# Kernel tuning notes

Hardware: AMD Instinct MI355X
Metric: run time of the kernel (lower is better)

## Reference

```python
import jax, jax.numpy as jnp
import numpy as np

B, T, C, F, E, K = 4, 2048, 1024, 4096, 8, 2
CAP_FACTOR = 1.0
AUX_COEF = 0.01
CAPACITY = max(1, int(CAP_FACTOR * (B * T) * max(1, K) / E + 0.9999))


def setup_inputs() -> dict:
    key = jax.random.key(0)
    ks = jax.random.split(key, 4)
    s = 0.02
    return {
        "x": jax.random.normal(ks[0], (B, T, C), jnp.float32),
        "w_gate": jax.random.normal(ks[1], (C, E), jnp.float32) * s,
        "b_gate": jnp.zeros((E,), jnp.float32),
        "W1": jax.random.normal(ks[2], (E, C, F), jnp.float32) * s,
        "b1": jnp.zeros((E, F), jnp.float32),
        "W2": jax.random.normal(ks[3], (E, F, C), jnp.float32) * s,
        "b2": jnp.zeros((E, C), jnp.float32),
    }


def reference(x, w_gate, b_gate, W1, b1, W2, b2):
    Bb, Tt, Cc = x.shape
    N = Bb * Tt
    S = N * K  # dispatch slots, token-major with k inner (matches the python double loop order)
    x_flat = x.reshape(N, Cc)

    # Top-K gating
    logits = x_flat @ w_gate + b_gate                       # [N, E]
    probs = jax.nn.softmax(logits, axis=-1)
    topk_w, topk_idx = jax.lax.top_k(probs, K)              # [N, K]
    topk_w = topk_w / (topk_w.sum(-1, keepdims=True) + 1e-9)

    e_flat = topk_idx.reshape(S)                            # expert id per slot
    w_flat = topk_w.reshape(S)
    tok = jnp.arange(S) // K                                # source token per slot

    # First-come-first-served capacity: position of each slot within its expert
    onehot = jax.nn.one_hot(e_flat, E, dtype=jnp.int32)     # [S, E]
    pos_in_e = (jnp.cumsum(onehot, axis=0) - onehot)        # exclusive count per expert
    pos_in_e = (pos_in_e * onehot).sum(-1)                  # [S]
    keep = pos_in_e < CAPACITY
    keepf = keep.astype(x.dtype)
    p_safe = jnp.where(keep, pos_in_e, CAPACITY - 1)        # dropped slots scatter zeros

    # Dispatch -> [E, capacity, C]
    disp = jnp.zeros((E, CAPACITY, Cc), x.dtype).at[e_flat, p_safe].add(
        x_flat[tok] * keepf[:, None]
    )

    # Per-expert FFN (grouped GEMM)
    h = jax.nn.gelu(jnp.einsum("epc,ecf->epf", disp, W1) + b1[:, None, :])
    y = jnp.einsum("epf,efc->epc", h, W2) + b2[:, None, :]  # [E, capacity, C]

    # Combine: gather each kept slot's expert output, weight, scatter-add back to tokens
    y_slot = y[e_flat, p_safe] * (w_flat * keepf)[:, None]  # [S, C]
    out = jnp.zeros((N, Cc), x.dtype).at[tok].add(y_slot).reshape(Bb, Tt, Cc)

    # Load-balancing aux loss (expert_load is detached in the original)
    expert_load = jnp.sum(onehot.astype(jnp.float32) * keepf[:, None], axis=0)  # [E]
    expert_load = jax.lax.stop_gradient(expert_load)
    frac_expected = probs.mean(axis=0)
    frac_expected = frac_expected / (frac_expected.sum() + 1e-9)
    frac_actual = expert_load / (expert_load.sum() + 1e-9)
    aux_loss = AUX_COEF * jnp.mean((frac_expected - frac_actual) ** 2)

    return out, aux_loss
```

## Files before the change

kernel.cpp:

```cpp
#include <hip/hip_runtime.h>
#include <hip/hip_bf16.h>
#include <math.h>


#define DEV __device__ __forceinline__

typedef __attribute__((ext_vector_type(4))) float f32x4;
typedef __attribute__((ext_vector_type(8))) short bf16x8;

constexpr int B_ = 4, T_ = 2048, C_ = 1024, F_ = 4096, E_ = 8, TOPK_ = 2;
constexpr int N_ = B_ * T_;
constexpr int S_ = N_ * TOPK_;
constexpr int CAP_ = 2048;

#define GLOAD16(G, L)                                              \
  __builtin_amdgcn_global_load_lds(                                \
      (const __attribute__((address_space(1))) void*)(G),          \
      (__attribute__((address_space(3))) void*)(L), 16, 0, 0)

DEV float gelu_tanh(float x) {
  float x3 = x * x * x;
  float u = 0.7978845608028654f * (x + 0.044715f * x3);
  return 0.5f * x * (1.0f + tanhf(u));
}


__global__ __launch_bounds__(256) void cvt_x_kernel(
    const float* __restrict__ in, __hip_bfloat16* __restrict__ out, int n4) {
  int i = blockIdx.x * 256 + threadIdx.x;
  if (i >= n4) return;
  float4 v = ((const float4*)in)[i];
  __hip_bfloat16 o[4] = {__float2bfloat16(v.x), __float2bfloat16(v.y),
                         __float2bfloat16(v.z), __float2bfloat16(v.w)};
  *(uint2*)(out + (size_t)i * 4) = *(uint2*)o;
}

__global__ __launch_bounds__(256) void transpose_cvt_kernel(
    const float* __restrict__ in, __hip_bfloat16* __restrict__ out, int R, int S) {
  __shared__ float tile[32][33];
  int e = blockIdx.z;
  int s0 = blockIdx.x * 32;
  int r0 = blockIdx.y * 32;
  int tx = threadIdx.x & 31;
  int ty = threadIdx.x >> 5;
  const float* ip = in + (size_t)e * R * S;
  __hip_bfloat16* op = out + (size_t)e * R * S;
#pragma unroll
  for (int i = 0; i < 32; i += 8)
    tile[ty + i][tx] = ip[(size_t)(r0 + ty + i) * S + s0 + tx];
  __syncthreads();
#pragma unroll
  for (int i = 0; i < 32; i += 8)
    op[(size_t)(s0 + ty + i) * R + r0 + tx] = __float2bfloat16(tile[tx][ty + i]);
}


__global__ __launch_bounds__(256) void gate_kernel(
    const float* __restrict__ x, const float* __restrict__ wg,
    const float* __restrict__ bg, int* __restrict__ slot_e,
    float* __restrict__ slot_w, float* __restrict__ probs_sum) {
  int lane = threadIdx.x & 63;
  int wv = threadIdx.x >> 6;
  int wid = blockIdx.x * 4 + wv;
  float psum[E_];
#pragma unroll
  for (int e = 0; e < E_; ++e) psum[e] = 0.f;

  for (int ti = 0; ti < 8; ++ti) {
    int t = wid * 8 + ti;
    const float* xr = x + (size_t)t * C_;
    float acc[E_];
#pragma unroll
    for (int e = 0; e < E_; ++e) acc[e] = 0.f;
    for (int c = lane; c < C_; c += 64) {
      float xv = xr[c];
      const float* wr = wg + (size_t)c * E_;
#pragma unroll
      for (int e = 0; e < E_; ++e) acc[e] += xv * wr[e];
    }
#pragma unroll
    for (int e = 0; e < E_; ++e) {
#pragma unroll
      for (int off = 32; off >= 1; off >>= 1)
        acc[e] += __shfl_xor(acc[e], off, 64);
    }
    if (lane == 0) {
      float lg[E_], p[E_];
      float mx = -1e30f;
#pragma unroll
      for (int e = 0; e < E_; ++e) { lg[e] = acc[e] + bg[e]; mx = fmaxf(mx, lg[e]); }
      float s = 0.f;
#pragma unroll
      for (int e = 0; e < E_; ++e) { p[e] = expf(lg[e] - mx); s += p[e]; }
      float inv = 1.f / s;
#pragma unroll
      for (int e = 0; e < E_; ++e) { p[e] *= inv; psum[e] += p[e]; }
      int i1 = 0; float p1 = p[0];
#pragma unroll
      for (int e = 1; e < E_; ++e) if (p[e] > p1) { p1 = p[e]; i1 = e; }
      int i2 = -1; float p2 = -1.f;
#pragma unroll
      for (int e = 0; e < E_; ++e) if (e != i1 && p[e] > p2) { p2 = p[e]; i2 = e; }
      float wden = 1.f / (p1 + p2 + 1e-9f);
      slot_e[2 * t] = i1;     slot_w[2 * t] = p1 * wden;
      slot_e[2 * t + 1] = i2; slot_w[2 * t + 1] = p2 * wden;
    }
  }
  if (lane == 0) {
#pragma unroll
    for (int e = 0; e < E_; ++e) atomicAdd(&probs_sum[e], psum[e]);
  }
}


__global__ __launch_bounds__(256) void scan_kernel(
    const int* __restrict__ slot_e, const float* __restrict__ slot_w,
    int* __restrict__ idx_list, float* __restrict__ w_list,
    const float* __restrict__ probs_sum, float* __restrict__ aux_out) {
  __shared__ int sc[256][E_];
  int tid = threadIdx.x;
  int s0 = tid * 64;
  int cnt[E_];
#pragma unroll
  for (int e = 0; e < E_; ++e) cnt[e] = 0;
  for (int j = 0; j < 64; ++j) cnt[slot_e[s0 + j]]++;
#pragma unroll
  for (int e = 0; e < E_; ++e) sc[tid][e] = cnt[e];
  __syncthreads();
  for (int off = 1; off < 256; off <<= 1) {
    int v[E_];
    bool act = (tid >= off);
    if (act) {
#pragma unroll
      for (int e = 0; e < E_; ++e) v[e] = sc[tid - off][e];
    }
    __syncthreads();
    if (act) {
#pragma unroll
      for (int e = 0; e < E_; ++e) sc[tid][e] += v[e];
    }
    __syncthreads();
  }
  int base[E_];
#pragma unroll
  for (int e = 0; e < E_; ++e) base[e] = tid ? sc[tid - 1][e] : 0;
  for (int j = 0; j < 64; ++j) {
    int s = s0 + j;
    int e = slot_e[s];
    int p = base[e]++;
    if (p < CAP_) {
      idx_list[e * CAP_ + p] = s >> 1;
      w_list[e * CAP_ + p] = slot_w[s];
    }
  }
  if (tid == 0) {
    float fe[E_], fa[E_], fs = 0.f, ls = 0.f;
#pragma unroll
    for (int e = 0; e < E_; ++e) {
      fe[e] = probs_sum[e] / (float)N_;
      fs += fe[e];
      int tot = sc[255][e];
      fa[e] = (float)(tot < CAP_ ? tot : CAP_);
      ls += fa[e];
    }
    float i1 = 1.f / (fs + 1e-9f), i2 = 1.f / (ls + 1e-9f);
    float a = 0.f;
#pragma unroll
    for (int e = 0; e < E_; ++e) {
      float d = fe[e] * i1 - fa[e] * i2;
      a += d * d;
    }
    aux_out[0] = 0.01f * a / (float)E_;
  }
}


template <int EPI, bool GATHER>
__global__ __launch_bounds__(256) void gemm_tile(
    const __hip_bfloat16* __restrict__ Aall,
    const __hip_bfloat16* __restrict__ Ball,
    const int* __restrict__ idxl,
    const float* __restrict__ wl,
    const float* __restrict__ bias,
    void* __restrict__ Cout,
    const __hip_bfloat16* __restrict__ zrow,
    int Ndim, int Kdim) {
  const int e = blockIdx.z;
  const int row0 = blockIdx.y * 128;
  const int col0 = blockIdx.x * 128;
  const int tid = threadIdx.x;
  const int lane = tid & 63;
  const int wv = tid >> 6;
  const int wm = wv >> 1, wn = wv & 1;

  __shared__ __align__(16) __hip_bfloat16 As[128 * 32];
  __shared__ __align__(16) __hip_bfloat16 Bs[128 * 32];

  const int rA0 = tid >> 2, kA0 = (tid & 3) * 8;
  const int rA1 = rA0 + 64;

  const __hip_bfloat16 *rowA0, *rowA1;
  if (GATHER) {
    int tok0 = idxl[e * CAP_ + row0 + rA0];
    int tok1 = idxl[e * CAP_ + row0 + rA1];
    rowA0 = (tok0 >= 0) ? Aall + (size_t)tok0 * Kdim : zrow;
    rowA1 = (tok1 >= 0) ? Aall + (size_t)tok1 * Kdim : zrow;
  } else {
    rowA0 = Aall + ((size_t)e * CAP_ + row0 + rA0) * Kdim;
    rowA1 = Aall + ((size_t)e * CAP_ + row0 + rA1) * Kdim;
  }
  const __hip_bfloat16* Be = Ball + (size_t)e * Ndim * Kdim;
  const __hip_bfloat16* rowB0 = Be + (size_t)(col0 + rA0) * Kdim;
  const __hip_bfloat16* rowB1 = Be + (size_t)(col0 + rA1) * Kdim;

  __hip_bfloat16* ldsA0 = As + (size_t)(wv * 64) * 8;
  __hip_bfloat16* ldsA1 = As + (size_t)(256 + wv * 64) * 8;
  __hip_bfloat16* ldsB0 = Bs + (size_t)(wv * 64) * 8;
  __hip_bfloat16* ldsB1 = Bs + (size_t)(256 + wv * 64) * 8;

  f32x4 acc[4][4];
#pragma unroll
  for (int m = 0; m < 4; ++m)
#pragma unroll
    for (int n = 0; n < 4; ++n) acc[m][n] = (f32x4){0.f, 0.f, 0.f, 0.f};

  const int rsel = lane & 15;
  const int ksel = (lane >> 4) * 8;

  for (int k0 = 0; k0 < Kdim; k0 += 32) {
    GLOAD16(rowA0 + k0 + kA0, ldsA0);
    GLOAD16(rowA1 + k0 + kA0, ldsA1);
    GLOAD16(rowB0 + k0 + kA0, ldsB0);
    GLOAD16(rowB1 + k0 + kA0, ldsB1);
    __syncthreads();

    bf16x8 af[4], bfv[4];
#pragma unroll
    for (int m = 0; m < 4; ++m)
      af[m] = *(const bf16x8*)(As + (wm * 64 + m * 16 + rsel) * 32 + ksel);
#pragma unroll
    for (int n = 0; n < 4; ++n)
      bfv[n] = *(const bf16x8*)(Bs + (wn * 64 + n * 16 + rsel) * 32 + ksel);
#pragma unroll
    for (int m = 0; m < 4; ++m)
#pragma unroll
      for (int n = 0; n < 4; ++n)
        acc[m][n] = __builtin_amdgcn_mfma_f32_16x16x32_bf16(af[m], bfv[n],
                                                            acc[m][n], 0, 0, 0);
    __syncthreads();
  }

  const float* brow = bias + (size_t)e * Ndim;
  const int orow0 = row0 + wm * 64 + (lane >> 4) * 4;
  const int ocol0 = col0 + wn * 64 + rsel;
  if (EPI == 0) {
    __hip_bfloat16* H = (__hip_bfloat16*)Cout + (size_t)e * CAP_ * Ndim;
#pragma unroll
    for (int m = 0; m < 4; ++m) {
#pragma unroll
      for (int n = 0; n < 4; ++n) {
        int cc = ocol0 + n * 16;
        float bv = brow[cc];
#pragma unroll
        for (int j = 0; j < 4; ++j) {
          int rr = orow0 + m * 16 + j;
          H[(size_t)rr * Ndim + cc] = __float2bfloat16(gelu_tanh(acc[m][n][j] + bv));
        }
      }
    }
  } else {
    float* out = (float*)Cout;
#pragma unroll
    for (int m = 0; m < 4; ++m) {
#pragma unroll
      for (int j = 0; j < 4; ++j) {
        int rr = orow0 + m * 16 + j;
        int t = idxl[e * CAP_ + rr];
        if (t < 0) continue;
        float w = wl[e * CAP_ + rr];
#pragma unroll
        for (int n = 0; n < 4; ++n) {
          int cc = ocol0 + n * 16;
          unsafeAtomicAdd(&out[(size_t)t * C_ + cc], w * (acc[m][n][j] + brow[cc]));
        }
      }
    }
  }
}


extern "C" void kernel_launch(void* const* d_in, const int* in_sizes, int n_in,
                              void* d_out, int out_size, void* d_ws,
                              size_t ws_size, hipStream_t stream) {
  (void)in_sizes; (void)n_in; (void)out_size; (void)ws_size;
  const float* x = (const float*)d_in[0];
  const float* w_gate = (const float*)d_in[1];
  const float* b_gate = (const float*)d_in[2];
  const float* W1 = (const float*)d_in[3];
  const float* b1 = (const float*)d_in[4];
  const float* W2 = (const float*)d_in[5];
  const float* b2 = (const float*)d_in[6];
  float* out = (float*)d_out;

  char* p = (char*)d_ws;
  __hip_bfloat16* xb = (__hip_bfloat16*)p;
  __hip_bfloat16* W1t = (__hip_bfloat16*)(p + ((size_t)16 << 20));
  __hip_bfloat16* W2t = (__hip_bfloat16*)p;
  __hip_bfloat16* Hb = (__hip_bfloat16*)(p + ((size_t)80 << 20));
  char* meta = p + ((size_t)208 << 20);
  int* slot_e = (int*)meta;
  float* slot_w = (float*)(meta + (64 << 10));
  int* idx_list = (int*)(meta + (128 << 10));
  float* w_list = (float*)(meta + (192 << 10));
  float* probs_sum = (float*)(meta + (256 << 10));
  __hip_bfloat16* zrow = (__hip_bfloat16*)(meta + (260 << 10));

  hipMemsetAsync(idx_list, 0xFF, E_ * CAP_ * sizeof(int), stream);
  hipMemsetAsync(probs_sum, 0, E_ * sizeof(float), stream);
  hipMemsetAsync(zrow, 0, 16 << 10, stream);
  hipMemsetAsync(out, 0, (size_t)N_ * C_ * sizeof(float), stream);

  cvt_x_kernel<<<(N_ * C_ / 4 + 255) / 256, 256, 0, stream>>>(x, xb, N_ * C_ / 4);
  transpose_cvt_kernel<<<dim3(F_ / 32, C_ / 32, E_), 256, 0, stream>>>(W1, W1t, C_, F_);
  gate_kernel<<<N_ / 32, 256, 0, stream>>>(x, w_gate, b_gate, slot_e, slot_w, probs_sum);
  scan_kernel<<<1, 256, 0, stream>>>(slot_e, slot_w, idx_list, w_list, probs_sum,
                                     out + (size_t)N_ * C_);
  gemm_tile<0, true><<<dim3(F_ / 128, CAP_ / 128, E_), 256, 0, stream>>>(
      xb, W1t, idx_list, nullptr, b1, Hb, zrow, F_, C_);
  transpose_cvt_kernel<<<dim3(C_ / 32, F_ / 32, E_), 256, 0, stream>>>(W2, W2t, F_, C_);
  gemm_tile<1, false><<<dim3(C_ / 128, CAP_ / 128, E_), 256, 0, stream>>>(
      Hb, W2t, idx_list, w_list, b2, out, zrow, C_, F_);
}
```

Before: 1.089 ms.

## Replace 128x128 grouped GEMM with double-buffered 256x256 tiles and swizzled LDS

Both expert GEMMs now use 256x256 output tiles with 512 threads and a K step of 64. Each wave computes 128x64 from double-buffered LDS, prefetching the next tile while MFMAs run on the current one. LDS reads use an XOR swizzle to avoid bank conflicts, wave priority is raised around the MFMA bursts, and a block-index remap places workgroups across XCDs. The aim is more data reuse per load and load latency hidden behind compute, at the cost of 128KB of LDS per block, higher register pressure, and fewer blocks per expert for the second GEMM.

```diff
diff --git a/kernel.cpp b/kernel.cpp
--- a/kernel.cpp
+++ b/kernel.cpp
@@ -176,7 +176,7 @@
 
 
 template <int EPI, bool GATHER>
-__global__ __launch_bounds__(256) void gemm_tile(
+__global__ __launch_bounds__(512, 2) void gemm256(
     const __hip_bfloat16* __restrict__ Aall,
     const __hip_bfloat16* __restrict__ Ball,
     const int* __restrict__ idxl,
@@ -184,107 +184,143 @@
     const float* __restrict__ bias,
     void* __restrict__ Cout,
     const __hip_bfloat16* __restrict__ zrow,
-    int Ndim, int Kdim) {
-  const int e = blockIdx.z;
-  const int row0 = blockIdx.y * 128;
-  const int col0 = blockIdx.x * 128;
+    int Ndim, int Kdim, int ncol) {
+  __shared__ __align__(16) __hip_bfloat16 lds[2][2][256 * 64];
+
+  const int nwg = gridDim.x;
+  const int wg = ((int)blockIdx.x & 7) * (nwg >> 3) + ((int)blockIdx.x >> 3);
+  const int e = wg / (ncol * 8);
+  const int rem = wg - e * (ncol * 8);
+  const int x = rem >> 3, y = rem & 7;
+  const int row0 = y * 256, col0 = x * 256;
+
   const int tid = threadIdx.x;
   const int lane = tid & 63;
-  const int wv = tid >> 6;
-  const int wm = wv >> 1, wn = wv & 1;
-
-  __shared__ __align__(16) __hip_bfloat16 As[128 * 32];
-  __shared__ __align__(16) __hip_bfloat16 Bs[128 * 32];
-
-  const int rA0 = tid >> 2, kA0 = (tid & 3) * 8;
-  const int rA1 = rA0 + 64;
-
-  const __hip_bfloat16 *rowA0, *rowA1;
-  if (GATHER) {
-    int tok0 = idxl[e * CAP_ + row0 + rA0];
-    int tok1 = idxl[e * CAP_ + row0 + rA1];
-    rowA0 = (tok0 >= 0) ? Aall + (size_t)tok0 * Kdim : zrow;
-    rowA1 = (tok1 >= 0) ? Aall + (size_t)tok1 * Kdim : zrow;
-  } else {
-    rowA0 = Aall + ((size_t)e * CAP_ + row0 + rA0) * Kdim;
-    rowA1 = Aall + ((size_t)e * CAP_ + row0 + rA1) * Kdim;
-  }
+  const int w = tid >> 6;
+  const int wm = w >> 2, wn = w & 3;
+
+  const int cb = ((lane & 7) * 16) ^ ((lane >> 5) << 5);
+  const int rch = w * 8 + (lane >> 3);
+  const __hip_bfloat16* srcA[4];
+  const __hip_bfloat16* srcB[4];
   const __hip_bfloat16* Be = Ball + (size_t)e * Ndim * Kdim;
-  const __hip_bfloat16* rowB0 = Be + (size_t)(col0 + rA0) * Kdim;
-  const __hip_bfloat16* rowB1 = Be + (size_t)(col0 + rA1) * Kdim;
-
-  __hip_bfloat16* ldsA0 = As + (size_t)(wv * 64) * 8;
-  __hip_bfloat16* ldsA1 = As + (size_t)(256 + wv * 64) * 8;
-  __hip_bfloat16* ldsB0 = Bs + (size_t)(wv * 64) * 8;
-  __hip_bfloat16* ldsB1 = Bs + (size_t)(256 + wv * 64) * 8;
-
-  f32x4 acc[4][4];
-#pragma unroll
-  for (int m = 0; m < 4; ++m)
-#pragma unroll
-    for (int n = 0; n < 4; ++n) acc[m][n] = (f32x4){0.f, 0.f, 0.f, 0.f};
-
-  const int rsel = lane & 15;
-  const int ksel = (lane >> 4) * 8;
-
-  for (int k0 = 0; k0 < Kdim; k0 += 32) {
-    GLOAD16(rowA0 + k0 + kA0, ldsA0);
-    GLOAD16(rowA1 + k0 + kA0, ldsA1);
-    GLOAD16(rowB0 + k0 + kA0, ldsB0);
-    GLOAD16(rowB1 + k0 + kA0, ldsB1);
-    __syncthreads();
-
-    bf16x8 af[4], bfv[4];
-#pragma unroll
-    for (int m = 0; m < 4; ++m)
-      af[m] = *(const bf16x8*)(As + (wm * 64 + m * 16 + rsel) * 32 + ksel);
-#pragma unroll
-    for (int n = 0; n < 4; ++n)
-      bfv[n] = *(const bf16x8*)(Bs + (wn * 64 + n * 16 + rsel) * 32 + ksel);
-#pragma unroll
-    for (int m = 0; m < 4; ++m)
-#pragma unroll
-      for (int n = 0; n < 4; ++n)
-        acc[m][n] = __builtin_amdgcn_mfma_f32_16x16x32_bf16(af[m], bfv[n],
-                                                            acc[m][n], 0, 0, 0);
-    __syncthreads();
-  }
+#pragma unroll
+  for (int c = 0; c < 4; ++c) {
+    int r = c * 64 + rch;
+    if (GATHER) {
+      int tok = idxl[e * CAP_ + row0 + r];
+      srcA[c] = ((tok >= 0) ? Aall + (size_t)tok * Kdim : zrow) + (cb >> 1);
+    } else {
+      srcA[c] = Aall + ((size_t)e * CAP_ + row0 + r) * Kdim + (cb >> 1);
+    }
+    srcB[c] = Be + (size_t)(col0 + r) * Kdim + (cb >> 1);
+  }
+  const int dstoff = w * 512;
+
+  const int sxor = (lane & 4) << 3;
+  const int rA = wm * 128 + (lane & 15);
+  const int rB = wn * 64 + (lane & 15);
+  const int kb = (lane >> 4) * 16;
+
+  f32x4 acc[8][4];
+#pragma unroll
+  for (int i = 0; i < 8; ++i)
+#pragma unroll
+    for (int j = 0; j < 4; ++j) acc[i][j] = (f32x4){0.f, 0.f, 0.f, 0.f};
+
+  const int NT = Kdim >> 6;
+
+#define STAGE_TILE(PAR, T)                                        \
+  {                                                               \
+    const int k0_ = (T) * 64;                                     \
+    _Pragma("unroll") for (int c = 0; c < 4; ++c) {               \
+      GLOAD16(srcA[c] + k0_, &lds[PAR][0][c * 4096 + dstoff]);    \
+      GLOAD16(srcB[c] + k0_, &lds[PAR][1][c * 4096 + dstoff]);    \
+    }                                                             \
+  }
+
+  STAGE_TILE(0, 0);
+  asm volatile("s_waitcnt vmcnt(0)" ::: "memory");
+  __builtin_amdgcn_sched_barrier(0);
+  __builtin_amdgcn_s_barrier();
+  __builtin_amdgcn_sched_barrier(0);
+
+  for (int t = 0; t < NT; ++t) {
+    const int par = t & 1;
+    const char* baseA = (const char*)&lds[par][0][0];
+    const char* baseB = (const char*)&lds[par][1][0];
+    bf16x8 bfr[4][2];
+#pragma unroll
+    for (int q = 0; q < 4; ++q) {
+      if (q == 0) {
+#pragma unroll
+        for (int n = 0; n < 4; ++n)
+#pragma unroll
+          for (int ks = 0; ks < 2; ++ks)
+            bfr[n][ks] = *(const bf16x8*)(
+                baseB + ((((rB + n * 16) * 128) + ks * 64 + kb) ^ sxor));
+      }
+      bf16x8 af[2][2];
+#pragma unroll
+      for (int i = 0; i < 2; ++i)
+#pragma unroll
+        for (int ks = 0; ks < 2; ++ks)
+          af[i][ks] = *(const bf16x8*)(
+              baseA + ((((rA + (q * 2 + i) * 16) * 128) + ks * 64 + kb) ^ sxor));
+      if (q == 0 && t + 1 < NT) STAGE_TILE(par ^ 1, t + 1);
+      __builtin_amdgcn_s_barrier();
+      __builtin_amdgcn_s_setprio(1);
+#pragma unroll
+      for (int ks = 0; ks < 2; ++ks)
+#pragma unroll
+        for (int i = 0; i < 2; ++i)
+#pragma unroll
+          for (int n = 0; n < 4; ++n)
+            acc[q * 2 + i][n] = __builtin_amdgcn_mfma_f32_16x16x32_bf16(
+                af[i][ks], bfr[n][ks], acc[q * 2 + i][n], 0, 0, 0);
+      __builtin_amdgcn_s_setprio(0);
+      __builtin_amdgcn_s_barrier();
+    }
+    asm volatile("s_waitcnt vmcnt(0)" ::: "memory");
+    __builtin_amdgcn_sched_barrier(0);
+    __builtin_amdgcn_s_barrier();
+    __builtin_amdgcn_sched_barrier(0);
+  }
+#undef STAGE_TILE
 
   const float* brow = bias + (size_t)e * Ndim;
-  const int orow0 = row0 + wm * 64 + (lane >> 4) * 4;
-  const int ocol0 = col0 + wn * 64 + rsel;
+  const int orow0 = row0 + wm * 128 + (lane >> 4) * 4;
+  const int ocol0 = col0 + wn * 64 + (lane & 15);
   if (EPI == 0) {
     __hip_bfloat16* H = (__hip_bfloat16*)Cout + (size_t)e * CAP_ * Ndim;
 #pragma unroll
-    for (int m = 0; m < 4; ++m) {
+    for (int mi = 0; mi < 8; ++mi)
 #pragma unroll
       for (int n = 0; n < 4; ++n) {
         int cc = ocol0 + n * 16;
         float bv = brow[cc];
 #pragma unroll
         for (int j = 0; j < 4; ++j) {
-          int rr = orow0 + m * 16 + j;
-          H[(size_t)rr * Ndim + cc] = __float2bfloat16(gelu_tanh(acc[m][n][j] + bv));
+          int rr = orow0 + mi * 16 + j;
+          H[(size_t)rr * Ndim + cc] = __float2bfloat16(gelu_tanh(acc[mi][n][j] + bv));
         }
       }
-    }
   } else {
-    float* out = (float*)Cout;
-#pragma unroll
-    for (int m = 0; m < 4; ++m) {
+    float* outp = (float*)Cout;
+#pragma unroll
+    for (int mi = 0; mi < 8; ++mi)
 #pragma unroll
       for (int j = 0; j < 4; ++j) {
-        int rr = orow0 + m * 16 + j;
-        int t = idxl[e * CAP_ + rr];
-        if (t < 0) continue;
-        float w = wl[e * CAP_ + rr];
+        int rr = orow0 + mi * 16 + j;
+        int tk = idxl[e * CAP_ + rr];
+        if (tk < 0) continue;
+        float ww = wl[e * CAP_ + rr];
 #pragma unroll
         for (int n = 0; n < 4; ++n) {
           int cc = ocol0 + n * 16;
-          unsafeAtomicAdd(&out[(size_t)t * C_ + cc], w * (acc[m][n][j] + brow[cc]));
+          unsafeAtomicAdd(&outp[(size_t)tk * C_ + cc], ww * (acc[mi][n][j] + brow[cc]));
         }
       }
-    }
   }
 }
 
@@ -325,9 +361,9 @@
   gate_kernel<<<N_ / 32, 256, 0, stream>>>(x, w_gate, b_gate, slot_e, slot_w, probs_sum);
   scan_kernel<<<1, 256, 0, stream>>>(slot_e, slot_w, idx_list, w_list, probs_sum,
                                      out + (size_t)N_ * C_);
-  gemm_tile<0, true><<<dim3(F_ / 128, CAP_ / 128, E_), 256, 0, stream>>>(
-      xb, W1t, idx_list, nullptr, b1, Hb, zrow, F_, C_);
+  gemm256<0, true><<<16 * 8 * E_, 512, 0, stream>>>(
+      xb, W1t, idx_list, nullptr, b1, Hb, zrow, F_, C_, 16);
   transpose_cvt_kernel<<<dim3(C_ / 32, F_ / 32, E_), 256, 0, stream>>>(W2, W2t, F_, C_);
-  gemm_tile<1, false><<<dim3(C_ / 128, CAP_ / 128, E_), 256, 0, stream>>>(
-      Hb, W2t, idx_list, w_list, b2, out, zrow, C_, F_);
-}
+  gemm256<1, false><<<4 * 8 * E_, 512, 0, stream>>>(
+      Hb, W2t, idx_list, w_list, b2, out, zrow, C_, F_, 4);
+}
```

After: 977.9 us. 10.2% less time.
